# Optimization experiments

Measured on AMD Instinct MI355X. Metric: run time of the kernel, lower is better.

## Reference

```python
import jax, jax.numpy as jnp
import numpy as np

T = 8388608  # number of timesteps

def setup_inputs() -> dict:
    key = jax.random.key(0)
    x = jax.random.normal(key, (T,), dtype=jnp.float32)
    return {
        "x": x,
        "x0": jnp.float32(0.0),   # initial state estimate
        "p0": jnp.float32(1.0),   # initial covariance
        "A": jnp.float32(0.98),   # state transition
        "H": jnp.float32(1.0),    # observation model
        "Q": jnp.float32(0.01),   # process noise
        "R": jnp.float32(0.1),    # observation noise
    }

def reference(x, x0, p0, A, H, Q, R):
    # Scalar Kalman filter recurrence over T timesteps, expressed as lax.scan.
    def step(carry, y):
        xs, ps = carry
        x_pred = A * xs
        P_pred = A * ps * A + Q
        K = P_pred * H / (H * P_pred * H + R)
        x_new = x_pred + K * (y - H * x_pred)
        p_new = P_pred - K * H * P_pred
        return (x_new, p_new), x_new

    _, esti = jax.lax.scan(step, (x0, p0), x)
    return esti.reshape(x.shape[0], 1)  # matches torch reshape(len_sample, -1)
```

## Files before the change

kernel.cpp:

```cpp
#include <hip/hip_runtime.h>


#define T_TOTAL 8388608
#define PER_WAVE 1024
#define WARM 64
#define NWAVES (T_TOTAL / PER_WAVE)
#define NBLOCKS (NWAVES / 4)
#define CONV_ITERS 40
#define PRE 128

__global__ __launch_bounds__(256) void kalman_kernel(
    const float* __restrict__ x,
    const float* __restrict__ x0p, const float* __restrict__ p0p,
    const float* __restrict__ Aip, const float* __restrict__ Hip,
    const float* __restrict__ Qip, const float* __restrict__ Rip,
    float* __restrict__ out)
{
  const int lane = threadIdx.x & 63;
  const int wid  = (blockIdx.x << 2) | (threadIdx.x >> 6);
  const long base = (long)wid * PER_WAVE;

  float ys[16];
  {
    const float* xp = x + base + (lane << 4);
    *(float4*)(ys + 0)  = *(const float4*)(xp + 0);
    *(float4*)(ys + 4)  = *(const float4*)(xp + 4);
    *(float4*)(ys + 8)  = *(const float4*)(xp + 8);
    *(float4*)(ys + 12) = *(const float4*)(xp + 12);
  }
  float yw = 0.0f;
  if (wid > 0) yw = x[base - WARM + lane];

  const float A = Aip[0], H = Hip[0], Q = Qip[0], R = Rip[0];

  float p = p0p[0];
  #pragma unroll 4
  for (int i = 0; i < CONV_ITERS; ++i) {
    float Pp = A * p * A + Q;
    float K  = Pp * H / (H * Pp * H + R);
    p = Pp - K * H * Pp;
  }
  const float PpI  = A * p * A + Q;
  const float kInf = PpI * H / (H * PpI * H + R);
  const float aInf = A * (1.0f - kInf * H);

  __shared__ float sA[PRE], sK[PRE];
  if (blockIdx.x == 0) {
    if (threadIdx.x < PRE) {
      float pp = p0p[0];
      for (int i = 0; i < (int)threadIdx.x; ++i) {
        float Pp = A * pp * A + Q;
        float K  = Pp * H / (H * Pp * H + R);
        pp = Pp - K * H * Pp;
      }
      float Pp = A * pp * A + Q;
      float K  = Pp * H / (H * Pp * H + R);
      sA[threadIdx.x] = A * (1.0f - K * H);
      sK[threadIdx.x] = K;
    }
    __syncthreads();
  }

  float carry;
  if (wid == 0) {
    carry = x0p[0];
  } else {
    float As = aInf, Bs = kInf * yw;
    #pragma unroll
    for (int off = 1; off < 64; off <<= 1) {
      float Au = __shfl_up(As, off);
      float Bu = __shfl_up(Bs, off);
      if (lane >= off) { Bs = As * Bu + Bs; As = As * Au; }
    }
    carry = __shfl(Bs, 63);
  }

  auto run = [&](auto coef) {
    float Ac = 1.0f, Bc = 0.0f;
    #pragma unroll
    for (int j = 0; j < 16; ++j) {
      float a, k; coef(j, a, k);
      Bc = a * Bc + k * ys[j];
      Ac = a * Ac;
    }
    float As = Ac, Bs = Bc;
    #pragma unroll
    for (int off = 1; off < 64; off <<= 1) {
      float Au = __shfl_up(As, off);
      float Bu = __shfl_up(Bs, off);
      if (lane >= off) { Bs = As * Bu + Bs; As = As * Au; }
    }
    const float Axp = __shfl_up(As, 1);
    const float Bxp = __shfl_up(Bs, 1);
    float r = (lane == 0) ? carry : (Axp * carry + Bxp);
    #pragma unroll
    for (int j = 0; j < 16; ++j) {
      float a, k; coef(j, a, k);
      r = a * r + k * ys[j];
      ys[j] = r;
    }
    float* op = out + base + (lane << 4);
    *(float4*)(op + 0)  = *(const float4*)(ys + 0);
    *(float4*)(op + 4)  = *(const float4*)(ys + 4);
    *(float4*)(op + 8)  = *(const float4*)(ys + 8);
    *(float4*)(op + 12) = *(const float4*)(ys + 12);
  };

  if (wid == 0) {
    run([&](int j, float& a, float& k) {
      int e = (lane << 4) + j;
      if (e < PRE) { a = sA[e]; k = sK[e]; }
      else         { a = aInf;  k = kInf;  }
    });
  } else {
    run([&](int j, float& a, float& k) { a = aInf; k = kInf; });
  }
}

extern "C" void kernel_launch(void* const* d_in, const int* in_sizes, int n_in,
                              void* d_out, int out_size, void* d_ws, size_t ws_size,
                              hipStream_t stream) {
  const float* x  = (const float*)d_in[0];
  const float* x0 = (const float*)d_in[1];
  const float* p0 = (const float*)d_in[2];
  const float* A  = (const float*)d_in[3];
  const float* H  = (const float*)d_in[4];
  const float* Q  = (const float*)d_in[5];
  const float* R  = (const float*)d_in[6];
  float* out = (float*)d_out;

  kalman_kernel<<<NBLOCKS, 256, 0, stream>>>(x, x0, p0, A, H, Q, R, out);
}
```

Before: 100.1 us.

## Use closed-form steady-state gain and simplify scan with scalar-only prefix

The steady-state covariance is now computed by solving the scalar Riccati equation in closed form, which removes the 40-iteration divide loop in every thread. The per-wave scan now carries only the additive term, with the multiplier given by precomputed powers of aInf, which halves the shuffle traffic. The warm-up carry becomes a weighted sum reduced with an xor-shuffle. Wave 0 runs an exact sequential filter for the first 64 steps in place of the 128-entry shared-memory coefficient table. Loads and stores are marked nontemporal and launch bounds request higher occupancy; outputs of wave 0 past step 64 rely on the gain having converged by then.

```diff
diff --git a/kernel.cpp b/kernel.cpp
--- a/kernel.cpp
+++ b/kernel.cpp
@@ -6,10 +6,26 @@
 #define WARM 64
 #define NWAVES (T_TOTAL / PER_WAVE)
 #define NBLOCKS (NWAVES / 4)
-#define CONV_ITERS 40
-#define PRE 128
 
-__global__ __launch_bounds__(256) void kalman_kernel(
+typedef float vfloat4 __attribute__((ext_vector_type(4)));
+
+__device__ __forceinline__ vfloat4 ntload4(const float* p) {
+  return __builtin_nontemporal_load((const vfloat4*)p);
+}
+__device__ __forceinline__ void ntstore4(float* p, vfloat4 v) {
+  __builtin_nontemporal_store(v, (vfloat4*)p);
+}
+__device__ __forceinline__ float pow_u6(float a, int e) {
+  float r = 1.0f, b = a;
+  #pragma unroll
+  for (int i = 0; i < 6; ++i) {
+    r = (e & (1 << i)) ? r * b : r;
+    b *= b;
+  }
+  return r;
+}
+
+__global__ __launch_bounds__(256, 4) void kalman_kernel(
     const float* __restrict__ x,
     const float* __restrict__ x0p, const float* __restrict__ p0p,
     const float* __restrict__ Aip, const float* __restrict__ Hip,
@@ -19,101 +35,90 @@
   const int lane = threadIdx.x & 63;
   const int wid  = (blockIdx.x << 2) | (threadIdx.x >> 6);
   const long base = (long)wid * PER_WAVE;
+  const float* xp = x + base + (lane << 4);
 
-  float ys[16];
-  {
-    const float* xp = x + base + (lane << 4);
-    *(float4*)(ys + 0)  = *(const float4*)(xp + 0);
-    *(float4*)(ys + 4)  = *(const float4*)(xp + 4);
-    *(float4*)(ys + 8)  = *(const float4*)(xp + 8);
-    *(float4*)(ys + 12) = *(const float4*)(xp + 12);
-  }
-  float yw = 0.0f;
-  if (wid > 0) yw = x[base - WARM + lane];
+  vfloat4 y0 = ntload4(xp);
+  vfloat4 y1 = ntload4(xp + 4);
+  vfloat4 y2 = ntload4(xp + 8);
+  vfloat4 y3 = ntload4(xp + 12);
+  float yw  = (wid > 0) ? x[base - WARM + lane] : 0.0f;
+  float xv0 = (wid == 0) ? x[lane] : 0.0f;
 
   const float A = Aip[0], H = Hip[0], Q = Qip[0], R = Rip[0];
+  const float x0 = x0p[0];
 
-  float p = p0p[0];
-  #pragma unroll 4
-  for (int i = 0; i < CONV_ITERS; ++i) {
-    float Pp = A * p * A + Q;
-    float K  = Pp * H / (H * Pp * H + R);
-    p = Pp - K * H * Pp;
-  }
-  const float PpI  = A * p * A + Q;
-  const float kInf = PpI * H / (H * PpI * H + R);
+  const float H2 = H * H;
+  const float b  = R * (1.0f - A * A) - Q * H2;
+  const float S  = (-b + sqrtf(b * b + 4.0f * H2 * Q * R)) / (2.0f * H2);
+  const float kInf = S * H / (H2 * S + R);
   const float aInf = A * (1.0f - kInf * H);
-
-  __shared__ float sA[PRE], sK[PRE];
-  if (blockIdx.x == 0) {
-    if (threadIdx.x < PRE) {
-      float pp = p0p[0];
-      for (int i = 0; i < (int)threadIdx.x; ++i) {
-        float Pp = A * pp * A + Q;
-        float K  = Pp * H / (H * Pp * H + R);
-        pp = Pp - K * H * Pp;
-      }
-      float Pp = A * pp * A + Q;
-      float K  = Pp * H / (H * Pp * H + R);
-      sA[threadIdx.x] = A * (1.0f - K * H);
-      sK[threadIdx.x] = K;
-    }
-    __syncthreads();
-  }
 
   float carry;
   if (wid == 0) {
-    carry = x0p[0];
+    carry = x0;
   } else {
-    float As = aInf, Bs = kInf * yw;
+    float v = kInf * pow_u6(aInf, 63 - lane) * yw;
     #pragma unroll
-    for (int off = 1; off < 64; off <<= 1) {
-      float Au = __shfl_up(As, off);
-      float Bu = __shfl_up(Bs, off);
-      if (lane >= off) { Bs = As * Bu + Bs; As = As * Au; }
-    }
-    carry = __shfl(Bs, 63);
+    for (int off = 32; off; off >>= 1) v += __shfl_xor(v, off);
+    carry = v;
   }
 
-  auto run = [&](auto coef) {
-    float Ac = 1.0f, Bc = 0.0f;
-    #pragma unroll
-    for (int j = 0; j < 16; ++j) {
-      float a, k; coef(j, a, k);
-      Bc = a * Bc + k * ys[j];
-      Ac = a * Ac;
-    }
-    float As = Ac, Bs = Bc;
-    #pragma unroll
-    for (int off = 1; off < 64; off <<= 1) {
-      float Au = __shfl_up(As, off);
-      float Bu = __shfl_up(Bs, off);
-      if (lane >= off) { Bs = As * Bu + Bs; As = As * Au; }
-    }
-    const float Axp = __shfl_up(As, 1);
-    const float Bxp = __shfl_up(Bs, 1);
-    float r = (lane == 0) ? carry : (Axp * carry + Bxp);
-    #pragma unroll
-    for (int j = 0; j < 16; ++j) {
-      float a, k; coef(j, a, k);
-      r = a * r + k * ys[j];
-      ys[j] = r;
-    }
-    float* op = out + base + (lane << 4);
-    *(float4*)(op + 0)  = *(const float4*)(ys + 0);
-    *(float4*)(op + 4)  = *(const float4*)(ys + 4);
-    *(float4*)(op + 8)  = *(const float4*)(ys + 8);
-    *(float4*)(op + 12) = *(const float4*)(ys + 12);
-  };
+  y0.x *= kInf; y0.y *= kInf; y0.z *= kInf; y0.w *= kInf;
+  y1.x *= kInf; y1.y *= kInf; y1.z *= kInf; y1.w *= kInf;
+  y2.x *= kInf; y2.y *= kInf; y2.z *= kInf; y2.w *= kInf;
+  y3.x *= kInf; y3.y *= kInf; y3.z *= kInf; y3.w *= kInf;
+
+  float Bs = y0.x;
+  Bs = aInf * Bs + y0.y;  Bs = aInf * Bs + y0.z;  Bs = aInf * Bs + y0.w;
+  Bs = aInf * Bs + y1.x;  Bs = aInf * Bs + y1.y;  Bs = aInf * Bs + y1.z;  Bs = aInf * Bs + y1.w;
+  Bs = aInf * Bs + y2.x;  Bs = aInf * Bs + y2.y;  Bs = aInf * Bs + y2.z;  Bs = aInf * Bs + y2.w;
+  Bs = aInf * Bs + y3.x;  Bs = aInf * Bs + y3.y;  Bs = aInf * Bs + y3.z;  Bs = aInf * Bs + y3.w;
+
+  const float a2 = aInf * aInf, a4 = a2 * a2, a8 = a4 * a4;
+  const float s16 = a8 * a8;
+  float f = s16;
+  #pragma unroll
+  for (int off = 1; off < 64; off <<= 1) {
+    float t = __shfl_up(Bs, off);
+    if (lane >= off) Bs = f * t + Bs;
+    f = f * f;
+  }
+
+  const float Bxp = __shfl_up(Bs, 1);
+  const float sl  = pow_u6(s16, lane);
+  float r = (lane == 0) ? carry : (sl * carry + Bxp);
+
+  r = aInf * r + y0.x; y0.x = r;  r = aInf * r + y0.y; y0.y = r;
+  r = aInf * r + y0.z; y0.z = r;  r = aInf * r + y0.w; y0.w = r;
+  r = aInf * r + y1.x; y1.x = r;  r = aInf * r + y1.y; y1.y = r;
+  r = aInf * r + y1.z; y1.z = r;  r = aInf * r + y1.w; y1.w = r;
+  r = aInf * r + y2.x; y2.x = r;  r = aInf * r + y2.y; y2.y = r;
+  r = aInf * r + y2.z; y2.z = r;  r = aInf * r + y2.w; y2.w = r;
+  r = aInf * r + y3.x; y3.x = r;  r = aInf * r + y3.y; y3.y = r;
+  r = aInf * r + y3.z; y3.z = r;  r = aInf * r + y3.w; y3.w = r;
+
+  float* op = out + base + (lane << 4);
+  if (wid != 0 || lane >= 4) {
+    ntstore4(op,      y0);
+    ntstore4(op + 4,  y1);
+    ntstore4(op + 8,  y2);
+    ntstore4(op + 12, y3);
+  }
 
   if (wid == 0) {
-    run([&](int j, float& a, float& k) {
-      int e = (lane << 4) + j;
-      if (e < PRE) { a = sA[e]; k = sK[e]; }
-      else         { a = aInf;  k = kInf;  }
-    });
-  } else {
-    run([&](int j, float& a, float& k) { a = aInf; k = kInf; });
+    float p  = p0p[0];
+    float xs = x0;
+    float keep = 0.0f;
+    for (int t = 0; t < WARM; ++t) {
+      const float yt = __shfl(xv0, t);
+      const float Pp = A * p * A + Q;
+      const float K  = Pp * H / (H * Pp * H + R);
+      const float xpred = A * xs;
+      xs = xpred + K * (yt - H * xpred);
+      if (t == lane) keep = xs;
+      p = Pp - K * H * Pp;
+    }
+    out[lane] = keep;
   }
 }
 
```

New measurement: 106.2 us. 6.1% more time.
